# Optimization experiments

Measured on AMD Instinct MI355X. Metric: run time of the kernel, lower is better.

The kernel has to match this reference:

```python
import jax, jax.numpy as jnp
import numpy as np

B, S, E, T, C, U, L = 2048, 50, 300, 8, 4, 300, 1000
NPAIR = E * (E - 1) // 2  # 44850
EPS = 1e-5


def setup_inputs() -> dict:
    key = jax.random.key(0)
    ks = jax.random.split(key, 18)
    r = lambda k, shape: jax.random.normal(k, shape, jnp.float32) * 0.05
    return {
        "x": jax.random.normal(ks[0], (B, S, E), jnp.float32),
        "label_embedding": jax.random.normal(ks[1], (L, U), jnp.float32),
        "fc1_w": r(ks[2], (T, E)), "fc1_b": r(ks[3], (T,)),
        "q1": jax.random.uniform(ks[4], (T,), jnp.float32),
        "fc3_w": r(ks[5], (T, E)), "fc3_b": r(ks[6], (T,)),
        "q2": jax.random.uniform(ks[7], (T,), jnp.float32),
        "fc5_w": r(ks[8], (E, 2 * E)), "fc5_b": r(ks[9], (E,)),
        "fc6_w": r(ks[10], (E, E)), "fc6_b": r(ks[11], (E,)),
        "fc7_w": r(ks[12], (E, NPAIR)), "fc7_b": r(ks[13], (E,)),
        "fc8_w": r(ks[14], (U, 2 * E)), "fc8_b": r(ks[15], (U,)),
        "v": jax.random.uniform(ks[16], (E, C), jnp.float32),
    }


def _bn(h, axes):
    # BatchNorm in training mode, fresh params (gamma=1, beta=0), biased var
    m = h.mean(axes, keepdims=True)
    var = h.var(axes, keepdims=True)
    return (h - m) * jax.lax.rsqrt(var + EPS)


def reference(x, label_embedding, fc1_w, fc1_b, q1, fc3_w, fc3_b, q2,
              fc5_w, fc5_b, fc6_w, fc6_b, fc7_w, fc7_b, fc8_w, fc8_b, v):
    pad = jnp.float32(-2 ** 32 + 1)
    sign = jnp.sign(jnp.sum(jnp.abs(x), axis=2))  # [B,S]

    def attn_pool(fw, fb, q):
        # fc -> relu -> BatchNorm1d(num_features=S) on [B,S,T] -> score -> softmax pool
        a = _bn(jax.nn.relu(jnp.einsum('bse,te->bst', x, fw) + fb), (0, 2))
        s = jnp.where(sign == 0, pad, a @ q)  # [B,S]
        w = jax.nn.softmax(s, axis=1)
        return jnp.einsum('bse,bs->be', x, w)  # [B,E]

    h = jnp.concatenate([attn_pool(fc1_w, fc1_b, q1),
                         attn_pool(fc3_w, fc3_b, q2)], axis=1)  # [B,2E]
    h5 = _bn(h @ fc5_w.T + fc5_b, (0,))       # [B,E]
    h6 = _bn(h5 @ fc6_w.T + fc6_b, (0,))      # [B,E]

    # CrossFeature: c[b,(i,j)] = h5[b,i]*h5[b,j]*(v_i . v_j), i<j row-major
    iu, ju = np.triu_indices(E, 1)
    g = jnp.sum(v[iu] * v[ju], axis=1)         # [NPAIR]
    cross = h5[:, iu] * h5[:, ju] * g          # [B,NPAIR]

    h7 = _bn(cross @ fc7_w.T + fc7_b, (0,))   # [B,E]
    out8 = jnp.concatenate([h6, h7], axis=1) @ fc8_w.T + fc8_b  # [B,U]
    return out8 @ label_embedding.T            # [B,L]
```

## Files before the change

### kernel.cpp

```cpp
#include <hip/hip_runtime.h>

#define B_ 2048
#define S_ 50
#define E_ 300
#define NPAIR 44850
#define KSPLIT 8
#define R_ (B_ * S_)
#define PADSCORE (-4294967295.0f)
#define RSBLK 512
#define RSROWS (B_ / RSBLK)

typedef _Float16 h8 __attribute__((ext_vector_type(8)));
typedef float f4 __attribute__((ext_vector_type(4)));

__global__ void k_meta(int* __restrict__ meta) {
  __shared__ int cnt[304], start[304];
  int i = threadIdx.x;
  if (i < 299) {
    int js = (i + 1) & ~7;
    cnt[i] = (300 - js + 31) >> 5;
  }
  __syncthreads();
  if (threadIdx.x == 0) {
    int s = 0;
    for (int r = 0; r < 299; r++) { start[r] = s; s += cnt[r]; }
  }
  __syncthreads();
  if (i < 299) {
    int js = (i + 1) & ~7;
    for (int c = 0; c < cnt[i]; c++)
      meta[start[i] + c] = i | ((js + 32 * c) << 16);
  }
}

__global__ __launch_bounds__(256) void k_wg3(
    const float* __restrict__ w7, const float* __restrict__ v,
    const int* __restrict__ meta, _Float16* __restrict__ Wgf) {
  __shared__ float gL[32];
  const int ch = blockIdx.x;
  const int mt = meta[ch];
  const int i = mt & 0xffff, j0 = mt >> 16;
  const int t = threadIdx.x;
  if (t < 32) {
    int j = j0 + t;
    float g = 0.f;
    if (j > i && j < 300)
      g = v[i*4+0]*v[j*4+0] + v[i*4+1]*v[j*4+1] + v[i*4+2]*v[j*4+2] + v[i*4+3]*v[j*4+3];
    gL[t] = g;
  }
  __syncthreads();
  const int grp = blockIdx.y * 4 + (t >> 6);
  const int lane = t & 63, l16 = lane & 15, quad = lane >> 4;
  const int e = grp * 16 + l16;
  const int ibase = i * (599 - i) / 2 - i - 1;
  h8 outv;
  #pragma unroll
  for (int tt = 0; tt < 8; tt++) {
    int k = quad * 8 + tt;
    int j = j0 + k;
    float val = 0.f;
    if (j > i && j < 300 && e < 300)
      val = w7[(size_t)e * NPAIR + ibase + j] * gL[k];
    outv[tt] = (_Float16)val;
  }
  *(h8*)&Wgf[(((size_t)ch * 20 + grp) * 64 + lane) * 8] = outv;
}

__global__ __launch_bounds__(256) void k_wf(
    const float* __restrict__ w, _Float16* __restrict__ Wf,
    int N, int K, int ngrp) {
  const int kt = blockIdx.x;
  const int grp = blockIdx.y * 4 + (threadIdx.x >> 6);
  const int lane = threadIdx.x & 63, l16 = lane & 15, quad = lane >> 4;
  const int e = grp * 16 + l16;
  if (grp >= ngrp) return;
  h8 o;
  #pragma unroll
  for (int tt = 0; tt < 8; tt++) {
    int k = kt * 32 + quad * 8 + tt;
    float val = (e < N && k < K) ? w[(size_t)e * K + k] : 0.f;
    o[tt] = (_Float16)val;
  }
  *(h8*)&Wf[(((size_t)kt * ngrp + grp) * 64 + lane) * 8] = o;
}

__global__ __launch_bounds__(256) void k_attn2(
    const float* __restrict__ x, const float* __restrict__ w1, const float* __restrict__ b1,
    const float* __restrict__ w3, const float* __restrict__ b3,
    float* __restrict__ a, float* __restrict__ sabs) {
  __shared__ float xs[128][68];
  __shared__ float wL[16][308];
  const int tid = threadIdx.x;
  const int r0 = blockIdx.x * 128;
  for (int u = tid; u < 16 * 75; u += 256) {
    int t = u / 75, q = u - t * 75;
    float4 v4 = (t < 8) ? *(const float4*)&w1[t * 300 + q * 4]
                        : *(const float4*)&w3[(t - 8) * 300 + q * 4];
    *(float4*)&wL[t][q * 4] = v4;
  }
  const int rg = tid >> 3, tg = tid & 7;
  float acc[4][2] = {};
  float sa[4] = {};
  for (int k0 = 0; k0 < 300; k0 += 64) {
    int w = min(64, 300 - k0);
    __syncthreads();
    #pragma unroll
    for (int it = 0; it < 8; it++) {
      int u = tid + it * 256;
      int r = u >> 4, q = u & 15;
      float4 v4 = {0.f, 0.f, 0.f, 0.f};
      if (q * 4 < w) v4 = *(const float4*)&x[(size_t)(r0 + r) * 300 + k0 + q * 4];
      *(float4*)&xs[r][q * 4] = v4;
    }
    __syncthreads();
    for (int q = 0; q < (w >> 2); q++) {
      float4 w0 = *(float4*)&wL[tg * 2][k0 + q * 4];
      float4 w1v = *(float4*)&wL[tg * 2 + 1][k0 + q * 4];
      #pragma unroll
      for (int k2 = 0; k2 < 4; k2++) {
        float4 xv = *(float4*)&xs[rg + 32 * k2][q * 4];
        acc[k2][0] += xv.x * w0.x + xv.y * w0.y + xv.z * w0.z + xv.w * w0.w;
        acc[k2][1] += xv.x * w1v.x + xv.y * w1v.y + xv.z * w1v.z + xv.w * w1v.w;
        if (tg == 0)
          sa[k2] += fabsf(xv.x) + fabsf(xv.y) + fabsf(xv.z) + fabsf(xv.w);
      }
    }
  }
  int t0 = tg * 2;
  float bb0 = (t0 < 8) ? b1[t0] : b3[t0 - 8];
  float bb1 = (t0 + 1 < 8) ? b1[t0 + 1] : b3[t0 + 1 - 8];
  #pragma unroll
  for (int k2 = 0; k2 < 4; k2++) {
    size_t r = r0 + rg + 32 * k2;
    a[r * 16 + t0]     = fmaxf(acc[k2][0] + bb0, 0.f);
    a[r * 16 + t0 + 1] = fmaxf(acc[k2][1] + bb1, 0.f);
    if (tg == 0) sabs[r] = sa[k2];
  }
}

__global__ void k_attnstats(const float* __restrict__ a, float* __restrict__ sstat) {
  int s = blockIdx.x, pool = blockIdx.y;
  float sum = 0.f, sq = 0.f;
  for (int b = threadIdx.x; b < B_; b += blockDim.x) {
    const float* row = &a[((size_t)b * S_ + s) * 16 + pool * 8];
    #pragma unroll
    for (int t = 0; t < 8; t++) { float v = row[t]; sum += v; sq += v * v; }
  }
  __shared__ float rs[2][4];
  int wave = threadIdx.x >> 6, lane = threadIdx.x & 63;
  #pragma unroll
  for (int off = 32; off; off >>= 1) { sum += __shfl_xor(sum, off); sq += __shfl_xor(sq, off); }
  if (lane == 0) { rs[0][wave] = sum; rs[1][wave] = sq; }
  __syncthreads();
  if (threadIdx.x == 0) {
    float S = rs[0][0] + rs[0][1] + rs[0][2] + rs[0][3];
    float Q = rs[1][0] + rs[1][1] + rs[1][2] + rs[1][3];
    float n = (float)(B_ * 8);
    float m = S / n;
    float var = Q / n - m * m;
    sstat[(pool * S_ + s) * 2 + 0] = m;
    sstat[(pool * S_ + s) * 2 + 1] = rsqrtf(var + 1e-5f);
  }
}

__global__ __launch_bounds__(256) void k_pool(
    const float* __restrict__ x, const float* __restrict__ a,
    const float* __restrict__ sabs, const float* __restrict__ sstat,
    const float* __restrict__ q1, const float* __restrict__ q2,
    _Float16* __restrict__ hh) {
  int b = blockIdx.x;
  __shared__ float w1s[S_], w2s[S_];
  int tid = threadIdx.x;
  if (tid < S_) {
    float sc1 = 0.f, sc2 = 0.f;
    const float* r1 = &a[((size_t)b * S_ + tid) * 16];
    const float* r2 = r1 + 8;
    float m1 = sstat[(0 * S_ + tid) * 2], rr1 = sstat[(0 * S_ + tid) * 2 + 1];
    float m2 = sstat[(1 * S_ + tid) * 2], rr2 = sstat[(1 * S_ + tid) * 2 + 1];
    #pragma unroll
    for (int t = 0; t < 8; t++) {
      sc1 += (r1[t] - m1) * rr1 * q1[t];
      sc2 += (r2[t] - m2) * rr2 * q2[t];
    }
    if (sabs[(size_t)b * S_ + tid] == 0.f) { sc1 = PADSCORE; sc2 = PADSCORE; }
    w1s[tid] = sc1; w2s[tid] = sc2;
  }
  __syncthreads();
  if (tid < 64) {
    float v1 = (tid < S_) ? w1s[tid] : -3.0e38f;
    float v2 = (tid < S_) ? w2s[tid] : -3.0e38f;
    float m1 = v1, m2 = v2;
    #pragma unroll
    for (int off = 32; off; off >>= 1) {
      m1 = fmaxf(m1, __shfl_xor(m1, off));
      m2 = fmaxf(m2, __shfl_xor(m2, off));
    }
    float e1 = (tid < S_) ? expf(v1 - m1) : 0.f;
    float e2 = (tid < S_) ? expf(v2 - m2) : 0.f;
    float s1 = e1, s2 = e2;
    #pragma unroll
    for (int off = 32; off; off >>= 1) { s1 += __shfl_xor(s1, off); s2 += __shfl_xor(s2, off); }
    if (tid < S_) { w1s[tid] = e1 / s1; w2s[tid] = e2 / s2; }
  }
  __syncthreads();
  for (int e = tid; e < E_; e += 256) {
    float p1 = 0.f, p2 = 0.f;
    for (int s = 0; s < S_; s++) {
      float xv = x[((size_t)b * S_ + s) * E_ + e];
      p1 += xv * w1s[s];
      p2 += xv * w2s[s];
    }
    hh[(size_t)b * 608 + e]       = (_Float16)p1;
    hh[(size_t)b * 608 + 300 + e] = (_Float16)p2;
  }
  if (tid < 8) hh[(size_t)b * 608 + 600 + tid] = (_Float16)0.f;
}

__global__ __launch_bounds__(256) void k_gemmf(
    const _Float16* __restrict__ Xh, int ldx,
    const _Float16* __restrict__ Wf, int ngrp,
    float* __restrict__ dst, int N,
    int nchunk, int cps) {
  __shared__ _Float16 XL[64][328];
  const int mblk = blockIdx.x, nblk = blockIdx.y, ks = blockIdx.z;
  const int tid = threadIdx.x;
  const int wave = tid >> 6, lane = tid & 63, quad = lane >> 4, l16 = lane & 15;
  const int wm = wave >> 1, wn = wave & 1;
  const int ck0 = ks * cps, ck1 = min(nchunk, ck0 + cps);
  const int ncol8 = (ck1 - ck0) * 4;
  {
    const _Float16* src = Xh + (size_t)mblk * 64 * ldx + ck0 * 32;
    for (int u = tid; u < 64 * ncol8; u += 256) {
      int r = u / ncol8, c8 = u - r * ncol8;
      *(h8*)&XL[r][c8 * 8] = *(const h8*)&src[(size_t)r * ldx + c8 * 8];
    }
  }
  __syncthreads();

  f4 acc[2][5];
  #pragma unroll
  for (int i = 0; i < 2; i++)
    #pragma unroll
    for (int j = 0; j < 5; j++) acc[i][j] = (f4){0.f, 0.f, 0.f, 0.f};

  const int gbase = nblk * 10 + wn * 5;
  const _Float16* wb = Wf + ((size_t)gbase * 64 + lane) * 8;
  h8 bA[5], bB[5];
  #define LOADB(DST, CH)                                                        \
    _Pragma("unroll")                                                           \
    for (int nt = 0; nt < 5; nt++)                                              \
      DST[nt] = (gbase + nt < ngrp)                                             \
          ? *(const h8*)&wb[((size_t)(CH) * ngrp + nt) * 512]                   \
          : (h8){0, 0, 0, 0, 0, 0, 0, 0};

  if (ck0 < ck1) { LOADB(bA, ck0); }
  if (ck0 + 1 < ck1) { LOADB(bB, ck0 + 1); }

  auto step = [&](int ch, h8* bf) {
    int c0 = (ch - ck0) * 32 + quad * 8;
    h8 af[2];
    #pragma unroll
    for (int mi = 0; mi < 2; mi++)
      af[mi] = *(const h8*)&XL[wm * 32 + mi * 16 + l16][c0];
    #pragma unroll
    for (int mi = 0; mi < 2; mi++)
      #pragma unroll
      for (int nt = 0; nt < 5; nt++)
        acc[mi][nt] = __builtin_amdgcn_mfma_f32_16x16x32_f16(af[mi], bf[nt], acc[mi][nt], 0, 0, 0);
  };

  int ch = ck0;
  while (ch < ck1) {
    step(ch, bA);
    if (ch + 2 < ck1) { LOADB(bA, ch + 2); }
    ch++;
    if (ch < ck1) {
      step(ch, bB);
      if (ch + 2 < ck1) { LOADB(bB, ch + 2); }
      ch++;
    }
  }
  #undef LOADB

  float* d = dst + (size_t)ks * ((size_t)B_ * N);
  #pragma unroll
  for (int mi = 0; mi < 2; mi++) {
    int b = mblk * 64 + wm * 32 + mi * 16 + quad * 4;
    #pragma unroll
    for (int nt = 0; nt < 5; nt++) {
      int e = (gbase + nt) * 16 + l16;
      if (e < N) {
        #pragma unroll
        for (int r = 0; r < 4; r++)
          d[(size_t)(b + r) * N + e] = acc[mi][nt][r];
      }
    }
  }
}

__global__ __launch_bounds__(256) void k_reduce_stat(
    const float* __restrict__ part, float* __restrict__ pre,
    float* __restrict__ cpart, int ksp) {
  int blk = blockIdx.x;
  int r0 = blk * RSROWS;
  for (int c = threadIdx.x; c < E_; c += 256) {
    float s = 0.f, q = 0.f;
    #pragma unroll
    for (int rr = 0; rr < RSROWS; rr++) {
      int r = r0 + rr;
      float v = 0.f;
      for (int k2 = 0; k2 < ksp; k2++)
        v += part[(size_t)k2 * (B_ * E_) + (size_t)r * E_ + c];
      pre[(size_t)r * E_ + c] = v;
      s += v; q += v * v;
    }
    cpart[((size_t)blk * E_ + c) * 2 + 0] = s;
    cpart[((size_t)blk * E_ + c) * 2 + 1] = q;
  }
}

__global__ __launch_bounds__(256) void k_colstat_fin(
    const float* __restrict__ part, float* __restrict__ stat,
    int N, int nparts, int M) {
  int c = blockIdx.x;
  if (c >= N) return;
  float s = 0.f, q = 0.f;
  for (int p = threadIdx.x; p < nparts; p += 256) {
    s += part[((size_t)p * N + c) * 2 + 0];
    q += part[((size_t)p * N + c) * 2 + 1];
  }
  #pragma unroll
  for (int off = 32; off; off >>= 1) { s += __shfl_xor(s, off); q += __shfl_xor(q, off); }
  __shared__ float rs[2][4];
  int wave = threadIdx.x >> 6, lane = threadIdx.x & 63;
  if (lane == 0) { rs[0][wave] = s; rs[1][wave] = q; }
  __syncthreads();
  if (threadIdx.x == 0) {
    float S = rs[0][0] + rs[0][1] + rs[0][2] + rs[0][3];
    float Q = rs[1][0] + rs[1][1] + rs[1][2] + rs[1][3];
    float m = S / (float)M;
    float var = Q / (float)M - m * m;
    stat[c * 2 + 0] = m;
    stat[c * 2 + 1] = rsqrtf(var + 1e-5f);
  }
}

__global__ void k_norm_h5h(const float* __restrict__ X, const float* __restrict__ stat,
                           _Float16* __restrict__ h5h) {
  int idx = blockIdx.x * 256 + threadIdx.x;
  if (idx >= B_ * 320) return;
  int b = idx / 320, c = idx - b * 320;
  if (c < E_) {
    float v = (X[(size_t)b * E_ + c] - stat[c * 2]) * stat[c * 2 + 1];
    h5h[idx] = (_Float16)v;
  } else {
    h5h[idx] = (_Float16)0.f;
  }
}

__global__ void k_norm_hcat(const float* __restrict__ X, const float* __restrict__ stat,
                            _Float16* __restrict__ Y, int off, int pad) {
  int W = 300 + pad;
  int idx = blockIdx.x * 256 + threadIdx.x;
  if (idx >= B_ * W) return;
  int b = idx / W, c = idx - b * W;
  if (c < 300) {
    float v = (X[(size_t)b * E_ + c] - stat[c * 2]) * stat[c * 2 + 1];
    Y[(size_t)b * 608 + off + c] = (_Float16)v;
  } else {
    Y[(size_t)b * 608 + 600 + (c - 300)] = (_Float16)0.f;
  }
}

__global__ void k_redbias_h(const float* __restrict__ part, const float* __restrict__ bias,
                            _Float16* __restrict__ out8h) {
  int idx = blockIdx.x * 256 + threadIdx.x;
  if (idx >= B_ * 320) return;
  int b = idx / 320, c = idx - b * 320;
  if (c < E_) {
    float s = bias[c];
    #pragma unroll
    for (int k2 = 0; k2 < 4; k2++)
      s += part[(size_t)k2 * (B_ * E_) + (size_t)b * E_ + c];
    out8h[idx] = (_Float16)s;
  } else {
    out8h[idx] = (_Float16)0.f;
  }
}

__global__ __launch_bounds__(256, 3) void k_bigmm4(
    const _Float16* __restrict__ Wgf, const _Float16* __restrict__ h5h,
    const int* __restrict__ meta, float* __restrict__ part,
    int nchunks, int cps) {
  __shared__ _Float16 h5L[64][328];
  __shared__ int metaL[200];
  const int ks = blockIdx.x, mblk = blockIdx.y, nblk = blockIdx.z;
  const int tid = threadIdx.x;
  const int wave = tid >> 6, lane = tid & 63, quad = lane >> 4, l16 = lane & 15;
  const int wm = wave >> 1, wn = wave & 1;
  const int ch0 = ks * cps;
  const int ch1 = min(nchunks, ch0 + cps);
  {
    const _Float16* src = h5h + (size_t)mblk * 64 * 320;
    for (int u = tid; u < 64 * 41; u += 256) {
      int r = u / 41, c8 = u - r * 41;
      h8 v8 = {0, 0, 0, 0, 0, 0, 0, 0};
      if (c8 < 40) v8 = *(const h8*)&src[r * 320 + c8 * 8];
      *(h8*)&h5L[r][c8 * 8] = v8;
    }
    for (int u = tid; u < 200; u += 256)
      metaL[u] = (u < cps && ch0 + u < nchunks) ? meta[ch0 + u] : 0;
  }
  __syncthreads();

  f4 acc[2][5];
  #pragma unroll
  for (int i = 0; i < 2; i++)
    #pragma unroll
    for (int j = 0; j < 5; j++) acc[i][j] = (f4){0.f, 0.f, 0.f, 0.f};

  const _Float16* wbase = Wgf + ((size_t)(nblk * 10 + wn * 5) * 64 + lane) * 8;
  h8 bA[5], bB[5];
  #define LOADB(DST, CH)                                                       \
    _Pragma("unroll")                                                          \
    for (int nt = 0; nt < 5; nt++)                                             \
      DST[nt] = *(const h8*)&wbase[(size_t)(CH) * 10240 + nt * 512];

  if (ch0 < ch1) { LOADB(bA, ch0); }
  if (ch0 + 1 < ch1) { LOADB(bB, ch0 + 1); }

  _Float16 hi[2];
  int iiprev = -1;

  auto step = [&](int ch, h8* bf) {
    const int mt = metaL[ch - ch0];
    const int ii = mt & 0xffff, j0 = mt >> 16;
    if (ii != iiprev) {
      #pragma unroll
      for (int mi = 0; mi < 2; mi++) hi[mi] = h5L[wm * 32 + mi * 16 + l16][ii];
      iiprev = ii;
    }
    h8 af[2];
    #pragma unroll
    for (int mi = 0; mi < 2; mi++) {
      h8 vj = *(const h8*)&h5L[wm * 32 + mi * 16 + l16][j0 + quad * 8];
      _Float16 h = hi[mi];
      h8 hs = {h, h, h, h, h, h, h, h};
      af[mi] = vj * hs;
    }
    #pragma unroll
    for (int mi = 0; mi < 2; mi++)
      #pragma unroll
      for (int nt = 0; nt < 5; nt++)
        acc[mi][nt] = __builtin_amdgcn_mfma_f32_16x16x32_f16(af[mi], bf[nt], acc[mi][nt], 0, 0, 0);
  };

  int ch = ch0;
  while (ch < ch1) {
    step(ch, bA);
    if (ch + 2 < ch1) { LOADB(bA, ch + 2); }
    ch++;
    if (ch < ch1) {
      step(ch, bB);
      if (ch + 2 < ch1) { LOADB(bB, ch + 2); }
      ch++;
    }
  }
  #undef LOADB

  float* dst = part + (size_t)ks * (B_ * E_);
  #pragma unroll
  for (int mi = 0; mi < 2; mi++) {
    int b = mblk * 64 + wm * 32 + mi * 16 + quad * 4;
    #pragma unroll
    for (int nt = 0; nt < 5; nt++) {
      int e = nblk * 160 + wn * 80 + nt * 16 + l16;
      if (e < E_) {
        #pragma unroll
        for (int r = 0; r < 4; r++)
          dst[(size_t)(b + r) * E_ + e] = acc[mi][nt][r];
      }
    }
  }
}

extern "C" void kernel_launch(void* const* d_in, const int* in_sizes, int n_in,
                              void* d_out, int out_size, void* d_ws, size_t ws_size,
                              hipStream_t stream) {
  const float* x    = (const float*)d_in[0];
  const float* lemb = (const float*)d_in[1];
  const float* fc1w = (const float*)d_in[2];
  const float* fc1b = (const float*)d_in[3];
  const float* q1   = (const float*)d_in[4];
  const float* fc3w = (const float*)d_in[5];
  const float* fc3b = (const float*)d_in[6];
  const float* q2   = (const float*)d_in[7];
  const float* fc5w = (const float*)d_in[8];
  const float* fc6w = (const float*)d_in[10];
  const float* fc7w = (const float*)d_in[12];
  const float* fc8w = (const float*)d_in[14];
  const float* fc8b = (const float*)d_in[15];
  const float* v    = (const float*)d_in[16];
  float* out = (float*)d_out;
  (void)in_sizes; (void)n_in; (void)out_size; (void)ws_size;

  int nchunks = 0;
  for (int i = 0; i < 299; i++) { int js = (i + 1) & ~7; nchunks += (300 - js + 31) >> 5; }
  int cps = (nchunks + KSPLIT - 1) / KSPLIT;

  char* base = (char*)d_ws;
  size_t off = 0;
  auto alloc = [&](size_t nbytes) -> char* {
    char* p = base + off;
    off = (off + nbytes + 255) & ~(size_t)255;
    return p;
  };
  int*       meta  = (int*)      alloc((size_t)nchunks * 4);
  _Float16*  Wgf   = (_Float16*) alloc((size_t)nchunks * 20 * 64 * 8 * 2);
  _Float16*  Wf5   = (_Float16*) alloc((size_t)19 * 19 * 512 * 2);
  _Float16*  Wf6   = (_Float16*) alloc((size_t)10 * 19 * 512 * 2);
  _Float16*  Wf8   = (_Float16*) alloc((size_t)19 * 19 * 512 * 2);
  _Float16*  WfL   = (_Float16*) alloc((size_t)10 * 63 * 512 * 2);
  _Float16*  hh    = (_Float16*) alloc((size_t)B_ * 608 * 2);
  _Float16*  h5h   = (_Float16*) alloc((size_t)B_ * 320 * 2);
  _Float16*  hcath = (_Float16*) alloc((size_t)B_ * 608 * 2);
  _Float16*  out8h = (_Float16*) alloc((size_t)B_ * 320 * 2);
  float*     pre   = (float*)    alloc((size_t)B_ * E_ * 4);
  float*     cpart = (float*)    alloc((size_t)RSBLK * E_ * 2 * 4);
  float*     cstat = (float*)    alloc((size_t)E_ * 2 * 4);
  size_t part_bytes = (size_t)KSPLIT * B_ * E_ * 4;
  char* scratch = alloc(part_bytes);
  float* a     = (float*)scratch;
  float* sabs  = a + (size_t)R_ * 16;
  float* sstat = sabs + R_;
  float* part  = (float*)scratch;

  hipLaunchKernelGGL(k_meta, dim3(1), dim3(320), 0, stream, meta);
  hipLaunchKernelGGL(k_wg3, dim3(nchunks, 5), dim3(256), 0, stream, fc7w, v, meta, Wgf);
  hipLaunchKernelGGL(k_wf, dim3(19, 5), dim3(256), 0, stream, fc5w, Wf5, 300, 600, 19);
  hipLaunchKernelGGL(k_wf, dim3(10, 5), dim3(256), 0, stream, fc6w, Wf6, 300, 300, 19);
  hipLaunchKernelGGL(k_wf, dim3(19, 5), dim3(256), 0, stream, fc8w, Wf8, 300, 600, 19);
  hipLaunchKernelGGL(k_wf, dim3(10, 16), dim3(256), 0, stream, lemb, WfL, 1000, 300, 63);
  hipLaunchKernelGGL(k_attn2, dim3(R_ / 128), dim3(256), 0, stream, x, fc1w, fc1b, fc3w, fc3b, a, sabs);
  hipLaunchKernelGGL(k_attnstats, dim3(S_, 2), dim3(256), 0, stream, a, sstat);
  hipLaunchKernelGGL(k_pool, dim3(B_), dim3(256), 0, stream, x, a, sabs, sstat, q1, q2, hh);
  hipLaunchKernelGGL(k_gemmf, dim3(32, 2, 4), dim3(256), 0, stream, hh, 608, Wf5, 19, part, 300, 19, 5);
  hipLaunchKernelGGL(k_reduce_stat, dim3(RSBLK), dim3(256), 0, stream, part, pre, cpart, 4);
  hipLaunchKernelGGL(k_colstat_fin, dim3(E_), dim3(256), 0, stream, cpart, cstat, E_, RSBLK, B_);
  hipLaunchKernelGGL(k_norm_h5h, dim3((B_ * 320) / 256), dim3(256), 0, stream, pre, cstat, h5h);
  hipLaunchKernelGGL(k_gemmf, dim3(32, 2, 4), dim3(256), 0, stream, h5h, 320, Wf6, 19, part, 300, 10, 3);
  hipLaunchKernelGGL(k_reduce_stat, dim3(RSBLK), dim3(256), 0, stream, part, pre, cpart, 4);
  hipLaunchKernelGGL(k_colstat_fin, dim3(E_), dim3(256), 0, stream, cpart, cstat, E_, RSBLK, B_);
  hipLaunchKernelGGL(k_norm_hcat, dim3((B_ * 300 + 255) / 256), dim3(256), 0, stream, pre, cstat, hcath, 0, 0);
  hipLaunchKernelGGL(k_bigmm4, dim3(KSPLIT, 32, 2), dim3(256), 0, stream, Wgf, h5h, meta, part, nchunks, cps);
  hipLaunchKernelGGL(k_reduce_stat, dim3(RSBLK), dim3(256), 0, stream, part, pre, cpart, 8);
  hipLaunchKernelGGL(k_colstat_fin, dim3(E_), dim3(256), 0, stream, cpart, cstat, E_, RSBLK, B_);
  hipLaunchKernelGGL(k_norm_hcat, dim3((B_ * 308 + 255) / 256), dim3(256), 0, stream, pre, cstat, hcath, 300, 8);
  hipLaunchKernelGGL(k_gemmf, dim3(32, 2, 4), dim3(256), 0, stream, hcath, 608, Wf8, 19, part, 300, 19, 5);
  hipLaunchKernelGGL(k_redbias_h, dim3((B_ * 320) / 256), dim3(256), 0, stream, part, fc8b, out8h);
  hipLaunchKernelGGL(k_gemmf, dim3(32, 7, 1), dim3(256), 0, stream, out8h, 320, WfL, 63, out, 1000, 10, 10);
}
```

Measured before the change: 519.1 us.

## Load GEMM A-fragments directly from global and raise split-K factors

```diff
diff --git a/kernel.cpp b/kernel.cpp
--- a/kernel.cpp
+++ b/kernel.cpp
@@ -4,7 +4,7 @@
 #define S_ 50
 #define E_ 300
 #define NPAIR 44850
-#define KSPLIT 8
+#define KSPLIT 12
 #define R_ (B_ * S_)
 #define PADSCORE (-4294967295.0f)
 #define RSBLK 512
@@ -221,21 +221,11 @@
     const _Float16* __restrict__ Wf, int ngrp,
     float* __restrict__ dst, int N,
     int nchunk, int cps) {
-  __shared__ _Float16 XL[64][328];
   const int mblk = blockIdx.x, nblk = blockIdx.y, ks = blockIdx.z;
   const int tid = threadIdx.x;
   const int wave = tid >> 6, lane = tid & 63, quad = lane >> 4, l16 = lane & 15;
   const int wm = wave >> 1, wn = wave & 1;
   const int ck0 = ks * cps, ck1 = min(nchunk, ck0 + cps);
-  const int ncol8 = (ck1 - ck0) * 4;
-  {
-    const _Float16* src = Xh + (size_t)mblk * 64 * ldx + ck0 * 32;
-    for (int u = tid; u < 64 * ncol8; u += 256) {
-      int r = u / ncol8, c8 = u - r * ncol8;
-      *(h8*)&XL[r][c8 * 8] = *(const h8*)&src[(size_t)r * ldx + c8 * 8];
-    }
-  }
-  __syncthreads();
 
   f4 acc[2][5];
   #pragma unroll
@@ -245,23 +235,23 @@
 
   const int gbase = nblk * 10 + wn * 5;
   const _Float16* wb = Wf + ((size_t)gbase * 64 + lane) * 8;
-  h8 bA[5], bB[5];
+  const _Float16* xb = Xh + (size_t)(mblk * 64 + wm * 32 + l16) * ldx + quad * 8;
+  h8 aA[2], aB[2], bA[5], bB[5];
   #define LOADB(DST, CH)                                                        \
     _Pragma("unroll")                                                           \
     for (int nt = 0; nt < 5; nt++)                                              \
       DST[nt] = (gbase + nt < ngrp)                                             \
           ? *(const h8*)&wb[((size_t)(CH) * ngrp + nt) * 512]                   \
           : (h8){0, 0, 0, 0, 0, 0, 0, 0};
-
-  if (ck0 < ck1) { LOADB(bA, ck0); }
-  if (ck0 + 1 < ck1) { LOADB(bB, ck0 + 1); }
-
-  auto step = [&](int ch, h8* bf) {
-    int c0 = (ch - ck0) * 32 + quad * 8;
-    h8 af[2];
-    #pragma unroll
-    for (int mi = 0; mi < 2; mi++)
-      af[mi] = *(const h8*)&XL[wm * 32 + mi * 16 + l16][c0];
+  #define LOADA(DST, CH)                                                        \
+    _Pragma("unroll")                                                           \
+    for (int mi = 0; mi < 2; mi++)                                              \
+      DST[mi] = *(const h8*)&xb[(size_t)mi * 16 * ldx + (CH) * 32];
+
+  if (ck0 < ck1) { LOADA(aA, ck0); LOADB(bA, ck0); }
+  if (ck0 + 1 < ck1) { LOADA(aB, ck0 + 1); LOADB(bB, ck0 + 1); }
+
+  auto step = [&](h8* af, h8* bf) {
     #pragma unroll
     for (int mi = 0; mi < 2; mi++)
       #pragma unroll
@@ -271,16 +261,17 @@
 
   int ch = ck0;
   while (ch < ck1) {
-    step(ch, bA);
-    if (ch + 2 < ck1) { LOADB(bA, ch + 2); }
+    step(aA, bA);
+    if (ch + 2 < ck1) { LOADA(aA, ch + 2); LOADB(bA, ch + 2); }
     ch++;
     if (ch < ck1) {
-      step(ch, bB);
-      if (ch + 2 < ck1) { LOADB(bB, ch + 2); }
+      step(aB, bB);
+      if (ch + 2 < ck1) { LOADA(aB, ch + 2); LOADB(bB, ch + 2); }
       ch++;
     }
   }
   #undef LOADB
+  #undef LOADA
 
   float* d = dst + (size_t)ks * ((size_t)B_ * N);
   #pragma unroll
@@ -373,14 +364,13 @@
 }
 
 __global__ void k_redbias_h(const float* __restrict__ part, const float* __restrict__ bias,
-                            _Float16* __restrict__ out8h) {
+                            _Float16* __restrict__ out8h, int ksp) {
   int idx = blockIdx.x * 256 + threadIdx.x;
   if (idx >= B_ * 320) return;
   int b = idx / 320, c = idx - b * 320;
   if (c < E_) {
     float s = bias[c];
-    #pragma unroll
-    for (int k2 = 0; k2 < 4; k2++)
+    for (int k2 = 0; k2 < ksp; k2++)
       s += part[(size_t)k2 * (B_ * E_) + (size_t)b * E_ + c];
     out8h[idx] = (_Float16)s;
   } else {
@@ -544,19 +534,19 @@
   hipLaunchKernelGGL(k_attn2, dim3(R_ / 128), dim3(256), 0, stream, x, fc1w, fc1b, fc3w, fc3b, a, sabs);
   hipLaunchKernelGGL(k_attnstats, dim3(S_, 2), dim3(256), 0, stream, a, sstat);
   hipLaunchKernelGGL(k_pool, dim3(B_), dim3(256), 0, stream, x, a, sabs, sstat, q1, q2, hh);
-  hipLaunchKernelGGL(k_gemmf, dim3(32, 2, 4), dim3(256), 0, stream, hh, 608, Wf5, 19, part, 300, 19, 5);
-  hipLaunchKernelGGL(k_reduce_stat, dim3(RSBLK), dim3(256), 0, stream, part, pre, cpart, 4);
+  hipLaunchKernelGGL(k_gemmf, dim3(32, 2, 8), dim3(256), 0, stream, hh, 608, Wf5, 19, part, 300, 19, 3);
+  hipLaunchKernelGGL(k_reduce_stat, dim3(RSBLK), dim3(256), 0, stream, part, pre, cpart, 8);
   hipLaunchKernelGGL(k_colstat_fin, dim3(E_), dim3(256), 0, stream, cpart, cstat, E_, RSBLK, B_);
   hipLaunchKernelGGL(k_norm_h5h, dim3((B_ * 320) / 256), dim3(256), 0, stream, pre, cstat, h5h);
-  hipLaunchKernelGGL(k_gemmf, dim3(32, 2, 4), dim3(256), 0, stream, h5h, 320, Wf6, 19, part, 300, 10, 3);
-  hipLaunchKernelGGL(k_reduce_stat, dim3(RSBLK), dim3(256), 0, stream, part, pre, cpart, 4);
+  hipLaunchKernelGGL(k_gemmf, dim3(32, 2, 8), dim3(256), 0, stream, h5h, 320, Wf6, 19, part, 300, 10, 2);
+  hipLaunchKernelGGL(k_reduce_stat, dim3(RSBLK), dim3(256), 0, stream, part, pre, cpart, 8);
   hipLaunchKernelGGL(k_colstat_fin, dim3(E_), dim3(256), 0, stream, cpart, cstat, E_, RSBLK, B_);
   hipLaunchKernelGGL(k_norm_hcat, dim3((B_ * 300 + 255) / 256), dim3(256), 0, stream, pre, cstat, hcath, 0, 0);
   hipLaunchKernelGGL(k_bigmm4, dim3(KSPLIT, 32, 2), dim3(256), 0, stream, Wgf, h5h, meta, part, nchunks, cps);
-  hipLaunchKernelGGL(k_reduce_stat, dim3(RSBLK), dim3(256), 0, stream, part, pre, cpart, 8);
+  hipLaunchKernelGGL(k_reduce_stat, dim3(RSBLK), dim3(256), 0, stream, part, pre, cpart, KSPLIT);
   hipLaunchKernelGGL(k_colstat_fin, dim3(E_), dim3(256), 0, stream, cpart, cstat, E_, RSBLK, B_);
   hipLaunchKernelGGL(k_norm_hcat, dim3((B_ * 308 + 255) / 256), dim3(256), 0, stream, pre, cstat, hcath, 300, 8);
-  hipLaunchKernelGGL(k_gemmf, dim3(32, 2, 4), dim3(256), 0, stream, hcath, 608, Wf8, 19, part, 300, 19, 5);
-  hipLaunchKernelGGL(k_redbias_h, dim3((B_ * 320) / 256), dim3(256), 0, stream, part, fc8b, out8h);
+  hipLaunchKernelGGL(k_gemmf, dim3(32, 2, 8), dim3(256), 0, stream, hcath, 608, Wf8, 19, part, 300, 19, 3);
+  hipLaunchKernelGGL(k_redbias_h, dim3((B_ * 320) / 256), dim3(256), 0, stream, part, fc8b, out8h, 8);
   hipLaunchKernelGGL(k_gemmf, dim3(32, 7, 1), dim3(256), 0, stream, out8h, 320, WfL, 63, out, 1000, 10, 10);
 }
```

Result: slower. 542.8 us (+4.6%).

## Reorganize cross-feature GEMM by j-column chunks with 128-row tiles and 16-way split

Applied to the files above, without the earlier changes.

```diff
diff --git a/kernel.cpp b/kernel.cpp
--- a/kernel.cpp
+++ b/kernel.cpp
@@ -4,33 +4,25 @@
 #define S_ 50
 #define E_ 300
 #define NPAIR 44850
-#define KSPLIT 8
 #define R_ (B_ * S_)
 #define PADSCORE (-4294967295.0f)
 #define RSBLK 512
 #define RSROWS (B_ / RSBLK)
 
+#define NPOS 1744
+#define BKSPLIT 16
+#define BCPS 112
+
 typedef _Float16 h8 __attribute__((ext_vector_type(8)));
 typedef float f4 __attribute__((ext_vector_type(4)));
 
 __global__ void k_meta(int* __restrict__ meta) {
-  __shared__ int cnt[304], start[304];
-  int i = threadIdx.x;
-  if (i < 299) {
-    int js = (i + 1) & ~7;
-    cnt[i] = (300 - js + 31) >> 5;
-  }
-  __syncthreads();
-  if (threadIdx.x == 0) {
-    int s = 0;
-    for (int r = 0; r < 299; r++) { start[r] = s; s += cnt[r]; }
-  }
-  __syncthreads();
-  if (i < 299) {
-    int js = (i + 1) & ~7;
-    for (int c = 0; c < cnt[i]; c++)
-      meta[start[i] + c] = i | ((js + 32 * c) << 16);
-  }
+  int pos = blockIdx.x * 256 + threadIdx.x;
+  if (pos >= NPOS) return;
+  int c = 0;
+  #pragma unroll
+  for (int cc = 1; cc < 10; cc++) if (pos >= 16 * cc * (cc + 1)) c = cc;
+  meta[pos] = (pos - 16 * c * (c + 1)) | ((c * 32) << 16);
 }
 
 __global__ __launch_bounds__(256) void k_wg3(
@@ -373,14 +365,13 @@
 }
 
 __global__ void k_redbias_h(const float* __restrict__ part, const float* __restrict__ bias,
-                            _Float16* __restrict__ out8h) {
+                            _Float16* __restrict__ out8h, int ksp) {
   int idx = blockIdx.x * 256 + threadIdx.x;
   if (idx >= B_ * 320) return;
   int b = idx / 320, c = idx - b * 320;
   if (c < E_) {
     float s = bias[c];
-    #pragma unroll
-    for (int k2 = 0; k2 < 4; k2++)
+    for (int k2 = 0; k2 < ksp; k2++)
       s += part[(size_t)k2 * (B_ * E_) + (size_t)b * E_ + c];
     out8h[idx] = (_Float16)s;
   } else {
@@ -388,93 +379,91 @@
   }
 }
 
-__global__ __launch_bounds__(256, 3) void k_bigmm4(
+__global__ __launch_bounds__(256, 2) void k_bigmm5(
     const _Float16* __restrict__ Wgf, const _Float16* __restrict__ h5h,
-    const int* __restrict__ meta, float* __restrict__ part,
-    int nchunks, int cps) {
-  __shared__ _Float16 h5L[64][328];
-  __shared__ int metaL[200];
-  const int ks = blockIdx.x, mblk = blockIdx.y, nblk = blockIdx.z;
+    float* __restrict__ part) {
+  const int n = blockIdx.x;
+  const int g = n & 31, mblk = n >> 5;
+  const int ks = g >> 1, nblk = g & 1;
   const int tid = threadIdx.x;
   const int wave = tid >> 6, lane = tid & 63, quad = lane >> 4, l16 = lane & 15;
   const int wm = wave >> 1, wn = wave & 1;
-  const int ch0 = ks * cps;
-  const int ch1 = min(nchunks, ch0 + cps);
-  {
-    const _Float16* src = h5h + (size_t)mblk * 64 * 320;
-    for (int u = tid; u < 64 * 41; u += 256) {
-      int r = u / 41, c8 = u - r * 41;
-      h8 v8 = {0, 0, 0, 0, 0, 0, 0, 0};
-      if (c8 < 40) v8 = *(const h8*)&src[r * 320 + c8 * 8];
-      *(h8*)&h5L[r][c8 * 8] = v8;
-    }
-    for (int u = tid; u < 200; u += 256)
-      metaL[u] = (u < cps && ch0 + u < nchunks) ? meta[ch0 + u] : 0;
-  }
-  __syncthreads();
-
-  f4 acc[2][5];
-  #pragma unroll
-  for (int i = 0; i < 2; i++)
+  const int pos0 = ks * BCPS;
+  const int pos1 = min(NPOS, pos0 + BCPS);
+
+  const int gbase = nblk * 10 + wn * 5;
+  const _Float16* wb = Wgf + ((size_t)gbase * 64 + lane) * 8;
+
+  const _Float16* rowp[4];
+  #pragma unroll
+  for (int mi = 0; mi < 4; mi++)
+    rowp[mi] = h5h + (size_t)(mblk * 128 + wm * 64 + mi * 16 + l16) * 320;
+
+  f4 acc[4][5];
+  #pragma unroll
+  for (int i = 0; i < 4; i++)
     #pragma unroll
     for (int j = 0; j < 5; j++) acc[i][j] = (f4){0.f, 0.f, 0.f, 0.f};
 
-  const _Float16* wbase = Wgf + ((size_t)(nblk * 10 + wn * 5) * 64 + lane) * 8;
-  h8 bA[5], bB[5];
-  #define LOADB(DST, CH)                                                       \
+  h8 bA[5], bB[5], vj[4];
+
+  #define LOADB5(DST, POS)                                                     \
     _Pragma("unroll")                                                          \
     for (int nt = 0; nt < 5; nt++)                                             \
-      DST[nt] = *(const h8*)&wbase[(size_t)(CH) * 10240 + nt * 512];
-
-  if (ch0 < ch1) { LOADB(bA, ch0); }
-  if (ch0 + 1 < ch1) { LOADB(bB, ch0 + 1); }
-
-  _Float16 hi[2];
-  int iiprev = -1;
-
-  auto step = [&](int ch, h8* bf) {
-    const int mt = metaL[ch - ch0];
-    const int ii = mt & 0xffff, j0 = mt >> 16;
-    if (ii != iiprev) {
+      DST[nt] = *(const h8*)&wb[(size_t)(POS) * 10240 + nt * 512];
+
+  int c = 0, cend = 32;
+  while (pos0 >= cend) { c++; cend = (c < 9) ? 16 * (c + 1) * (c + 2) : NPOS; }
+  int cumc = 16 * c * (c + 1);
+  #pragma unroll
+  for (int mi = 0; mi < 4; mi++)
+    vj[mi] = *(const h8*)&rowp[mi][c * 32 + quad * 8];
+
+  LOADB5(bA, pos0);
+  LOADB5(bB, pos0 + 1);
+
+  #define STEP5(BUF, T)                                                        \
+    _Pragma("unroll")                                                          \
+    for (int mi = 0; mi < 4; mi++) {                                           \
+      _Float16 hsc = hi8[mi][T];                                               \
+      h8 hs = {hsc, hsc, hsc, hsc, hsc, hsc, hsc, hsc};                        \
+      h8 af = vj[mi] * hs;                                                     \
+      _Pragma("unroll")                                                        \
+      for (int nt = 0; nt < 5; nt++)                                           \
+        acc[mi][nt] = __builtin_amdgcn_mfma_f32_16x16x32_f16(af, BUF[nt], acc[mi][nt], 0, 0, 0); \
+    }
+
+  for (int p = pos0; p < pos1; p += 8) {
+    if (p >= cend) {
+      do { c++; cend = (c < 9) ? 16 * (c + 1) * (c + 2) : NPOS; } while (p >= cend);
+      cumc = 16 * c * (c + 1);
       #pragma unroll
-      for (int mi = 0; mi < 2; mi++) hi[mi] = h5L[wm * 32 + mi * 16 + l16][ii];
-      iiprev = ii;
-    }
-    h8 af[2];
-    #pragma unroll
-    for (int mi = 0; mi < 2; mi++) {
-      h8 vj = *(const h8*)&h5L[wm * 32 + mi * 16 + l16][j0 + quad * 8];
-      _Float16 h = hi[mi];
-      h8 hs = {h, h, h, h, h, h, h, h};
-      af[mi] = vj * hs;
-    }
-    #pragma unroll
-    for (int mi = 0; mi < 2; mi++)
-      #pragma unroll
-      for (int nt = 0; nt < 5; nt++)
-        acc[mi][nt] = __builtin_amdgcn_mfma_f32_16x16x32_f16(af[mi], bf[nt], acc[mi][nt], 0, 0, 0);
-  };
-
-  int ch = ch0;
-  while (ch < ch1) {
-    step(ch, bA);
-    if (ch + 2 < ch1) { LOADB(bA, ch + 2); }
-    ch++;
-    if (ch < ch1) {
-      step(ch, bB);
-      if (ch + 2 < ch1) { LOADB(bB, ch + 2); }
-      ch++;
-    }
-  }
-  #undef LOADB
+      for (int mi = 0; mi < 4; mi++)
+        vj[mi] = *(const h8*)&rowp[mi][c * 32 + quad * 8];
+    }
+    const int i0 = p - cumc;
+    h8 hi8[4];
+    #pragma unroll
+    for (int mi = 0; mi < 4; mi++)
+      hi8[mi] = *(const h8*)&rowp[mi][i0];
+
+    #pragma unroll
+    for (int t = 0; t < 8; t += 2) {
+      STEP5(bA, t);     LOADB5(bA, p + t + 2);
+      STEP5(bB, t + 1); LOADB5(bB, p + t + 3);
+    }
+  }
+  #undef LOADB5
+  #undef STEP5
 
   float* dst = part + (size_t)ks * (B_ * E_);
-  #pragma unroll
-  for (int mi = 0; mi < 2; mi++) {
-    int b = mblk * 64 + wm * 32 + mi * 16 + quad * 4;
+  const int b0 = mblk * 128 + wm * 64;
+  #pragma unroll
+  for (int mi = 0; mi < 4; mi++) {
+    int b = b0 + mi * 16 + quad * 4;
     #pragma unroll
     for (int nt = 0; nt < 5; nt++) {
-      int e = nblk * 160 + wn * 80 + nt * 16 + l16;
+      int e = (gbase + nt) * 16 + l16;
       if (e < E_) {
         #pragma unroll
         for (int r = 0; r < 4; r++)
@@ -504,10 +493,6 @@
   float* out = (float*)d_out;
   (void)in_sizes; (void)n_in; (void)out_size; (void)ws_size;
 
-  int nchunks = 0;
-  for (int i = 0; i < 299; i++) { int js = (i + 1) & ~7; nchunks += (300 - js + 31) >> 5; }
-  int cps = (nchunks + KSPLIT - 1) / KSPLIT;
-
   char* base = (char*)d_ws;
   size_t off = 0;
   auto alloc = [&](size_t nbytes) -> char* {
@@ -515,8 +500,8 @@
     off = (off + nbytes + 255) & ~(size_t)255;
     return p;
   };
-  int*       meta  = (int*)      alloc((size_t)nchunks * 4);
-  _Float16*  Wgf   = (_Float16*) alloc((size_t)nchunks * 20 * 64 * 8 * 2);
+  int*       meta  = (int*)      alloc((size_t)NPOS * 4);
+  _Float16*  Wgf   = (_Float16*) alloc((size_t)(NPOS + 8) * 20 * 64 * 8 * 2);
   _Float16*  Wf5   = (_Float16*) alloc((size_t)19 * 19 * 512 * 2);
   _Float16*  Wf6   = (_Float16*) alloc((size_t)10 * 19 * 512 * 2);
   _Float16*  Wf8   = (_Float16*) alloc((size_t)19 * 19 * 512 * 2);
@@ -528,15 +513,15 @@
   float*     pre   = (float*)    alloc((size_t)B_ * E_ * 4);
   float*     cpart = (float*)    alloc((size_t)RSBLK * E_ * 2 * 4);
   float*     cstat = (float*)    alloc((size_t)E_ * 2 * 4);
-  size_t part_bytes = (size_t)KSPLIT * B_ * E_ * 4;
+  size_t part_bytes = (size_t)BKSPLIT * B_ * E_ * 4;
   char* scratch = alloc(part_bytes);
   float* a     = (float*)scratch;
   float* sabs  = a + (size_t)R_ * 16;
   float* sstat = sabs + R_;
   float* part  = (float*)scratch;
 
-  hipLaunchKernelGGL(k_meta, dim3(1), dim3(320), 0, stream, meta);
-  hipLaunchKernelGGL(k_wg3, dim3(nchunks, 5), dim3(256), 0, stream, fc7w, v, meta, Wgf);
+  hipLaunchKernelGGL(k_meta, dim3((NPOS + 255) / 256), dim3(256), 0, stream, meta);
+  hipLaunchKernelGGL(k_wg3, dim3(NPOS, 5), dim3(256), 0, stream, fc7w, v, meta, Wgf);
   hipLaunchKernelGGL(k_wf, dim3(19, 5), dim3(256), 0, stream, fc5w, Wf5, 300, 600, 19);
   hipLaunchKernelGGL(k_wf, dim3(10, 5), dim3(256), 0, stream, fc6w, Wf6, 300, 300, 19);
   hipLaunchKernelGGL(k_wf, dim3(19, 5), dim3(256), 0, stream, fc8w, Wf8, 300, 600, 19);
@@ -552,11 +537,11 @@
   hipLaunchKernelGGL(k_reduce_stat, dim3(RSBLK), dim3(256), 0, stream, part, pre, cpart, 4);
   hipLaunchKernelGGL(k_colstat_fin, dim3(E_), dim3(256), 0, stream, cpart, cstat, E_, RSBLK, B_);
   hipLaunchKernelGGL(k_norm_hcat, dim3((B_ * 300 + 255) / 256), dim3(256), 0, stream, pre, cstat, hcath, 0, 0);
-  hipLaunchKernelGGL(k_bigmm4, dim3(KSPLIT, 32, 2), dim3(256), 0, stream, Wgf, h5h, meta, part, nchunks, cps);
-  hipLaunchKernelGGL(k_reduce_stat, dim3(RSBLK), dim3(256), 0, stream, part, pre, cpart, 8);
+  hipLaunchKernelGGL(k_bigmm5, dim3(BKSPLIT * 32), dim3(256), 0, stream, Wgf, h5h, part);
+  hipLaunchKernelGGL(k_reduce_stat, dim3(RSBLK), dim3(256), 0, stream, part, pre, cpart, BKSPLIT);
   hipLaunchKernelGGL(k_colstat_fin, dim3(E_), dim3(256), 0, stream, cpart, cstat, E_, RSBLK, B_);
   hipLaunchKernelGGL(k_norm_hcat, dim3((B_ * 308 + 255) / 256), dim3(256), 0, stream, pre, cstat, hcath, 300, 8);
   hipLaunchKernelGGL(k_gemmf, dim3(32, 2, 4), dim3(256), 0, stream, hcath, 608, Wf8, 19, part, 300, 19, 5);
-  hipLaunchKernelGGL(k_redbias_h, dim3((B_ * 320) / 256), dim3(256), 0, stream, part, fc8b, out8h);
+  hipLaunchKernelGGL(k_redbias_h, dim3((B_ * 320) / 256), dim3(256), 0, stream, part, fc8b, out8h, 4);
   hipLaunchKernelGGL(k_gemmf, dim3(32, 7, 1), dim3(256), 0, stream, out8h, 320, WfL, 63, out, 1000, 10, 10);
 }
```

New measurement: 526.0 us. No clear change (+1.3%).
